# Optimization experiments

Hardware: AMD Instinct MI355X
Metric: run time of the kernel (lower is better)

Reference implementation:

```python
import jax, jax.numpy as jnp
import numpy as np

H = 768
NH = 12
HD = H // NH
NDIM = 5
LN_EPS = 1e-5


def setup_inputs() -> dict:
    key = jax.random.key(0)
    ks = jax.random.split(key, 12)
    B, S = 4, 2048
    xavier = lambda k: jax.random.uniform(k, (H, H), jnp.float32, -1.0, 1.0) * np.sqrt(6.0 / (H + H))
    return {
        "hidden_states": jax.random.normal(ks[0], (B, S, H), jnp.float32),
        "Wq": xavier(ks[1]), "bq": jnp.zeros((H,), jnp.float32),
        "Wk": xavier(ks[2]), "bk": jnp.zeros((H,), jnp.float32),
        "Wv": xavier(ks[3]), "bv": jnp.zeros((H,), jnp.float32),
        "Wo": xavier(ks[4]), "bo": jnp.zeros((H,), jnp.float32),
        # per-dimension, per-head scalar biases (torch init: zeros; use small randn so grads are non-trivial)
        "dim_biases": 0.02 * jax.random.normal(ks[5], (NDIM, NH), jnp.float32),
        "ln_gamma": jnp.ones((H,), jnp.float32),
        "ln_beta": jnp.zeros((H,), jnp.float32),
        "attention_mask": jax.random.randint(ks[6], (4, 2048), 0, 2, jnp.int32),
        "dimension_idx": 2,
    }


def reference(hidden_states, Wq, bq, Wk, bk, Wv, bv, Wo, bo, dim_biases,
              ln_gamma, ln_beta, attention_mask, dimension_idx):
    B, S, _ = hidden_states.shape
    residual = hidden_states
    # torch nn.Linear: x @ W.T + b
    q = (hidden_states @ Wq.T + bq).reshape(B, S, NH, HD).transpose(0, 2, 1, 3)  # [B,NH,S,HD]
    k = (hidden_states @ Wk.T + bk).reshape(B, S, NH, HD).transpose(0, 2, 1, 3)
    v = (hidden_states @ Wv.T + bv).reshape(B, S, NH, HD).transpose(0, 2, 1, 3)

    scores = jnp.einsum("bhqd,bhkd->bhqk", q, k) / np.sqrt(HD)  # [B,NH,S,S]
    if dimension_idx is not None and dimension_idx < NDIM:
        scores = scores + dim_biases[dimension_idx][None, :, None, None]
    # mask over key positions, broadcast over heads and queries
    scores = jnp.where(attention_mask[:, None, None, :] == 0, -jnp.inf, scores)
    attn = jax.nn.softmax(scores, axis=-1)

    ctx = jnp.einsum("bhqk,bhkd->bhqd", attn, v)  # [B,NH,S,HD]
    ctx = ctx.transpose(0, 2, 1, 3).reshape(B, S, H)
    out = ctx @ Wo.T + bo

    y = out + residual
    mu = jnp.mean(y, axis=-1, keepdims=True)
    var = jnp.var(y, axis=-1, keepdims=True)
    y = (y - mu) / jnp.sqrt(var + LN_EPS) * ln_gamma + ln_beta
    return y
```

## Files before the change

kernel.cpp:

```cpp
#include <hip/hip_runtime.h>
#include <hip/hip_bf16.h>

#define HH    768
#define NHEAD 12
#define HDIM  64
#define BB    4
#define SS    2048
#define MM    (BB*SS)
#define NDIMS 5
#define WEL   (HH*HH)
#define LOG2E 1.44269504088896f
#define QSCALE 0.180336881f

typedef unsigned short u16;
typedef __attribute__((ext_vector_type(8))) short short8;
typedef __attribute__((ext_vector_type(4))) float floatx4;
typedef __attribute__((ext_vector_type(16))) float floatx16;
typedef __attribute__((ext_vector_type(4))) unsigned int uint4v;
typedef __attribute__((ext_vector_type(2))) unsigned int uint2v;

__device__ __forceinline__ float bf2f(u16 u) {
    return __uint_as_float(((unsigned int)u) << 16);
}
__device__ __forceinline__ u16 f2bf(float f) {
    unsigned int x = __float_as_uint(f);
    unsigned int r = (x + 0x7fffu + ((x >> 16) & 1u)) >> 16;
    return (u16)r;
}
__device__ __forceinline__ unsigned int pack_bf16x2(float a, float b) {
    float2 f2 = make_float2(a, b);
    __hip_bfloat162 h2 = __float22bfloat162_rn(f2);
    return *reinterpret_cast<unsigned int*>(&h2);
}
__device__ __forceinline__ void gld16(const u16* g, u16* l) {
    __builtin_amdgcn_global_load_lds(
        (const __attribute__((address_space(1))) unsigned int*)g,
        (__attribute__((address_space(3))) unsigned int*)l, 16, 0, 0);
}

__global__ __launch_bounds__(256) void f32_to_bf16(
    const float* __restrict__ in, u16* __restrict__ out, int n8)
{
    int i = blockIdx.x * 256 + threadIdx.x;
    if (i >= n8) return;
    float4 a = ((const float4*)in)[i*2];
    float4 b = ((const float4*)in)[i*2 + 1];
    ushort4 lo, hi;
    lo.x = f2bf(a.x); lo.y = f2bf(a.y); lo.z = f2bf(a.z); lo.w = f2bf(a.w);
    hi.x = f2bf(b.x); hi.y = f2bf(b.y); hi.z = f2bf(b.z); hi.w = f2bf(b.w);
    ((ushort4*)out)[i*2]     = lo;
    ((ushort4*)out)[i*2 + 1] = hi;
}

#define XCVT_BLKS ((MM*HH)/8/256)
#define WCVT_BLKS (WEL/8/256)
__global__ __launch_bounds__(256) void cvt_all(
    const float* __restrict__ x,
    const float* __restrict__ W0, const float* __restrict__ W1,
    const float* __restrict__ W2, const float* __restrict__ W3,
    u16* __restrict__ xb, u16* __restrict__ wb)
{
    const int bid = blockIdx.x;
    const float* src;
    u16* dst;
    int i;
    if (bid < XCVT_BLKS) {
        src = x; dst = xb; i = bid * 256 + threadIdx.x;
    } else {
        const int wsel = (bid - XCVT_BLKS) / WCVT_BLKS;
        src = (wsel == 0) ? W0 : (wsel == 1) ? W1 : (wsel == 2) ? W2 : W3;
        dst = wb + (size_t)wsel * WEL;
        i = ((bid - XCVT_BLKS) % WCVT_BLKS) * 256 + threadIdx.x;
    }
    float4 a = ((const float4*)src)[i*2];
    float4 b = ((const float4*)src)[i*2 + 1];
    ushort4 lo, hi;
    lo.x = f2bf(a.x); lo.y = f2bf(a.y); lo.z = f2bf(a.z); lo.w = f2bf(a.w);
    hi.x = f2bf(b.x); hi.y = f2bf(b.y); hi.z = f2bf(b.z); hi.w = f2bf(b.w);
    ((ushort4*)dst)[i*2]     = lo;
    ((ushort4*)dst)[i*2 + 1] = hi;
}

__global__ __launch_bounds__(256) void v_transpose(
    const u16* __restrict__ V, u16* __restrict__ vt)
{
    __shared__ unsigned Ls[64][36];
    const int t = threadIdx.x;
    const int kt = blockIdx.x, h = blockIdx.y, b = blockIdx.z;
    const int p  = t & 31;
    const int dg = (t >> 5) * 8;
    const u16* va = V + ((size_t)(b*SS + kt*64 + 2*p))*HH + h*HDIM + dg;
    const u16* vb = va + HH;
    uint4 A = *(const uint4*)va;
    uint4 Bv = *(const uint4*)vb;
    const unsigned* Aw = (const unsigned*)&A;
    const unsigned* Bw = (const unsigned*)&Bv;
    #pragma unroll
    for (int i = 0; i < 4; ++i) {
        unsigned a = Aw[i], c = Bw[i];
        Ls[dg + 2*i][p]     = (a & 0xffffu) | (c << 16);
        Ls[dg + 2*i + 1][p] = (a >> 16) | (c & 0xffff0000u);
    }
    __syncthreads();
    const int d = t >> 2, kc = (t & 3) * 8;
    uint4 o0 = *(const uint4*)&Ls[d][kc];
    uint4 o1 = *(const uint4*)&Ls[d][kc + 4];
    u16* dst = vt + ((size_t)((b*NHEAD + h)*HDIM + d))*SS + kt*64 + kc*2;
    *(uint4*)dst       = o0;
    *(uint4*)(dst + 8) = o1;
}

__global__ __launch_bounds__(256, 3) void gemm_gld_qkv(
    const u16* __restrict__ Xb, const u16* __restrict__ Wb3,
    const float* __restrict__ bq, const float* __restrict__ bk, const float* __restrict__ bv,
    u16* __restrict__ oq, u16* __restrict__ ok, u16* __restrict__ vt)
{
    __shared__ u16 Xs[128][64];
    __shared__ u16 Ws[192][64];
    const int t = threadIdx.x;
    const int w = t >> 6, lane = t & 63;
    const int wy = w >> 1, wx = w & 1;
    const int m = lane & 31, hh = lane >> 5;
    const int grow = lane >> 3;
    const int cg   = (lane & 7) ^ grow;

    const int flat = blockIdx.x + 12 * blockIdx.y;
    const int swz  = (flat & 7) * 96 + (flat >> 3);
    const int j0 = (swz % 12) * 192;
    const int i0 = (swz / 12) * 128;
    const int sel = j0 / HH;
    const int lj  = j0 - sel * HH;
    const float* biasL = ((sel == 0) ? bq : (sel == 1) ? bk : bv) + lj;
    const u16* Wrows = Wb3 + (size_t)j0 * HH;

    floatx16 acc[2][3];
    #pragma unroll
    for (int am = 0; am < 2; ++am)
        #pragma unroll
        for (int bn = 0; bn < 3; ++bn)
            #pragma unroll
            for (int r = 0; r < 16; ++r) acc[am][bn][r] = 0.f;

    if (sel != 2) {
        for (int k0 = 0; k0 < HH; k0 += 64) {
            __syncthreads();
            #pragma unroll
            for (int j = 0; j < 4; ++j) {
                const int r = w*32 + j*8;
                gld16(Xb + (size_t)(i0 + r + grow)*HH + k0 + cg*8, &Xs[r][0]);
            }
            #pragma unroll
            for (int j = 0; j < 6; ++j) {
                const int r = w*48 + j*8;
                gld16(Wrows + (size_t)(r + grow)*HH + k0 + cg*8, &Ws[r][0]);
            }
            __syncthreads();

            #pragma unroll
            for (int kh = 0; kh < 4; ++kh) {
                const int ch = kh*2 + hh;
                short8 af[2], bf[3];
                #pragma unroll
                for (int am = 0; am < 2; ++am)
                    af[am] = *(const short8*)&Xs[wy*64 + am*32 + m][(ch ^ (m & 7))*8];
                #pragma unroll
                for (int bn = 0; bn < 3; ++bn)
                    bf[bn] = *(const short8*)&Ws[wx*96 + bn*32 + m][(ch ^ (m & 7))*8];
                #pragma unroll
                for (int am = 0; am < 2; ++am)
                    #pragma unroll
                    for (int bn = 0; bn < 3; ++bn)
                        acc[am][bn] = __builtin_amdgcn_mfma_f32_32x32x16_bf16(
                            af[am], bf[bn], acc[am][bn], 0, 0, 0);
            }
        }

        u16* outL = ((sel == 0) ? oq : ok) + lj;
        float bb[3];
        #pragma unroll
        for (int bn = 0; bn < 3; ++bn) bb[bn] = biasL[wx*96 + bn*32 + m];
        #pragma unroll
        for (int am = 0; am < 2; ++am)
            #pragma unroll
            for (int bn = 0; bn < 3; ++bn)
                #pragma unroll
                for (int r = 0; r < 16; ++r) {
                    int row = i0 + wy*64 + am*32 + (r & 3) + 8*(r >> 2) + 4*hh;
                    outL[(size_t)row*HH + wx*96 + bn*32 + m] = f2bf(acc[am][bn][r] + bb[bn]);
                }
    } else {
        for (int k0 = 0; k0 < HH; k0 += 64) {
            __syncthreads();
            #pragma unroll
            for (int j = 0; j < 4; ++j) {
                const int r = w*32 + j*8;
                gld16(Xb + (size_t)(i0 + r + grow)*HH + k0 + cg*8, &Xs[r][0]);
            }
            #pragma unroll
            for (int j = 0; j < 6; ++j) {
                const int r = w*48 + j*8;
                gld16(Wrows + (size_t)(r + grow)*HH + k0 + cg*8, &Ws[r][0]);
            }
            __syncthreads();

            #pragma unroll
            for (int kh = 0; kh < 4; ++kh) {
                const int ch = kh*2 + hh;
                short8 af[2], bf[3];
                #pragma unroll
                for (int am = 0; am < 2; ++am)
                    af[am] = *(const short8*)&Xs[wy*64 + am*32 + m][(ch ^ (m & 7))*8];
                #pragma unroll
                for (int bn = 0; bn < 3; ++bn)
                    bf[bn] = *(const short8*)&Ws[wx*96 + bn*32 + m][(ch ^ (m & 7))*8];
                #pragma unroll
                for (int am = 0; am < 2; ++am)
                    #pragma unroll
                    for (int bn = 0; bn < 3; ++bn)
                        acc[am][bn] = __builtin_amdgcn_mfma_f32_32x32x16_bf16(
                            bf[bn], af[am], acc[am][bn], 0, 0, 0);
            }
        }

        const int b_ = i0 / SS;
        const int key0 = (i0 % SS) + wy*64 + m;
        #pragma unroll
        for (int am = 0; am < 2; ++am)
            #pragma unroll
            for (int bn = 0; bn < 3; ++bn)
                #pragma unroll
                for (int qq = 0; qq < 4; ++qq) {
                    float4 bv4 = *(const float4*)&biasL[wx*96 + bn*32 + qq*8 + 4*hh];
                    const float* bvp = (const float*)&bv4;
                    #pragma unroll
                    for (int j = 0; j < 4; ++j) {
                        const int r = qq*4 + j;
                        const int wcol = wx*96 + bn*32 + qq*8 + 4*hh + j;
                        vt[(size_t)(b_*HH + lj + wcol)*SS + key0 + am*32] =
                            f2bf(acc[am][bn][r] + bvp[j]);
                    }
                }
    }
}

__global__ __launch_bounds__(256) void gemm_gld_m64(
    const u16* __restrict__ Xb, const u16* __restrict__ Wb,
    const float* __restrict__ bias, u16* __restrict__ out)
{
    __shared__ u16 Xs[64][64];
    __shared__ u16 Ws[128][64];
    const int t = threadIdx.x;
    const int w = t >> 6, lane = t & 63;
    const int m = lane & 31, hh = lane >> 5;
    const int grow = lane >> 3;
    const int cg   = (lane & 7) ^ grow;

    const int flat = blockIdx.x + 6 * blockIdx.y;
    const int swz  = (flat & 7) * 96 + (flat >> 3);
    const int j0 = (swz % 6) * 128;
    const int i0 = (swz / 6) * 64;

    floatx16 acc[2];
    #pragma unroll
    for (int am = 0; am < 2; ++am)
        #pragma unroll
        for (int r = 0; r < 16; ++r) acc[am][r] = 0.f;

    for (int k0 = 0; k0 < HH; k0 += 64) {
        __syncthreads();
        #pragma unroll
        for (int j = 0; j < 2; ++j) {
            const int r = w*16 + j*8;
            gld16(Xb + (size_t)(i0 + r + grow)*HH + k0 + cg*8, &Xs[r][0]);
        }
        #pragma unroll
        for (int j = 0; j < 4; ++j) {
            const int r = w*32 + j*8;
            gld16(Wb + (size_t)(j0 + r + grow)*HH + k0 + cg*8, &Ws[r][0]);
        }
        __syncthreads();

        #pragma unroll
        for (int kh = 0; kh < 4; ++kh) {
            const int ch = kh*2 + hh;
            short8 af[2], bf;
            af[0] = *(const short8*)&Xs[m][(ch ^ (m & 7))*8];
            af[1] = *(const short8*)&Xs[32 + m][(ch ^ (m & 7))*8];
            bf    = *(const short8*)&Ws[w*32 + m][(ch ^ (m & 7))*8];
            acc[0] = __builtin_amdgcn_mfma_f32_32x32x16_bf16(af[0], bf, acc[0], 0, 0, 0);
            acc[1] = __builtin_amdgcn_mfma_f32_32x32x16_bf16(af[1], bf, acc[1], 0, 0, 0);
        }
    }

    const float bb = bias[j0 + w*32 + m];
    #pragma unroll
    for (int am = 0; am < 2; ++am)
        #pragma unroll
        for (int r = 0; r < 16; ++r) {
            int row = i0 + am*32 + (r & 3) + 8*(r >> 2) + 4*hh;
            out[(size_t)row*HH + j0 + w*32 + m] = f2bf(acc[am][r] + bb);
        }
}

__global__ __launch_bounds__(256) void gemm_mfma_nt(
    const u16* __restrict__ Xb, const float* __restrict__ W,
    const float* __restrict__ bias, u16* __restrict__ out)
{
    __shared__ u16 Xs[128][40];
    __shared__ u16 Wt[64][40];
    const int t = threadIdx.x;
    const int w = t >> 6, lane = t & 63;
    const int c = lane & 15, qd = lane >> 4;
    const int i0 = blockIdx.y * 128, j0 = blockIdx.x * 64;
    const int xrow = t >> 1, xoff = (t & 1) * 16;
    const int wn = t >> 2, woff = (t & 3) * 8;

    floatx4 acc[2][4];
    #pragma unroll
    for (int mt = 0; mt < 2; ++mt)
        #pragma unroll
        for (int nt = 0; nt < 4; ++nt) acc[mt][nt] = (floatx4){0.f,0.f,0.f,0.f};

    for (int k0 = 0; k0 < HH; k0 += 32) {
        uint4 xa  = *(const uint4*)(Xb + (size_t)(i0 + xrow)*HH + k0 + xoff);
        uint4 xb2 = *(const uint4*)(Xb + (size_t)(i0 + xrow)*HH + k0 + xoff + 8);
        float4 wa = *(const float4*)(W + (size_t)(j0 + wn)*HH + k0 + woff);
        float4 wb = *(const float4*)(W + (size_t)(j0 + wn)*HH + k0 + woff + 4);
        __syncthreads();
        *(uint4*)&Xs[xrow][xoff]     = xa;
        *(uint4*)&Xs[xrow][xoff + 8] = xb2;
        ushort4 w0, w1;
        w0.x = f2bf(wa.x); w0.y = f2bf(wa.y); w0.z = f2bf(wa.z); w0.w = f2bf(wa.w);
        w1.x = f2bf(wb.x); w1.y = f2bf(wb.y); w1.z = f2bf(wb.z); w1.w = f2bf(wb.w);
        *(ushort4*)&Wt[wn][woff]     = w0;
        *(ushort4*)&Wt[wn][woff + 4] = w1;
        __syncthreads();

        short8 a0 = *(const short8*)&Xs[w*32 + c][qd*8];
        short8 a1 = *(const short8*)&Xs[w*32 + 16 + c][qd*8];
        #pragma unroll
        for (int nt = 0; nt < 4; ++nt) {
            short8 bfr = *(const short8*)&Wt[nt*16 + c][qd*8];
            acc[0][nt] = __builtin_amdgcn_mfma_f32_16x16x32_bf16(a0, bfr, acc[0][nt], 0, 0, 0);
            acc[1][nt] = __builtin_amdgcn_mfma_f32_16x16x32_bf16(a1, bfr, acc[1][nt], 0, 0, 0);
        }
    }

    float bv[4];
    #pragma unroll
    for (int nt = 0; nt < 4; ++nt) bv[nt] = bias[j0 + nt*16 + c];
    #pragma unroll
    for (int mt = 0; mt < 2; ++mt)
        #pragma unroll
        for (int nt = 0; nt < 4; ++nt)
            #pragma unroll
            for (int r = 0; r < 4; ++r)
                out[(size_t)(i0 + w*32 + mt*16 + qd*4 + r)*HH + j0 + nt*16 + c] =
                    f2bf(acc[mt][nt][r] + bv[nt]);
}

__global__ __launch_bounds__(256, 3) void attn_mfma32(
    const u16* __restrict__ Q, const u16* __restrict__ K, const u16* __restrict__ vt,
    const float* __restrict__ dim_biases, const int* __restrict__ mask,
    const int* __restrict__ dim_idx_p, u16* __restrict__ ctx)
{
    __shared__ u16 Ks[2][64][64];
    __shared__ u16 Vs[2][64][64];
    __shared__ float madd[2][64];

    const int t = threadIdx.x;
    const int w = t >> 6, lane = t & 63;
    const int ql = lane & 31, hi = lane >> 5;
    const int sw7 = ql & 7;

    const int flat = blockIdx.x + 16 * (blockIdx.y + 12 * blockIdx.z);
    const int swz  = (flat & 7) * 96 + (flat >> 3);
    const int q0 = (swz & 15) * 128;
    const int h  = (swz >> 4) % NHEAD;
    const int b  = swz / (16 * NHEAD);

    const int didx = *dim_idx_p;
    const float db2 = ((didx < NDIMS) ? dim_biases[didx*NHEAD + h] : 0.f) * LOG2E;

    const int grow = lane >> 3;
    const int cg   = (lane & 7) ^ grow;

    const u16* Vrows = vt + (size_t)(b*NHEAD + h)*HDIM*SS;

    short8 ones;
    #pragma unroll
    for (int j = 0; j < 8; ++j) ones[j] = (short)0x3F80;

    short8 qv[4];
    {
        const u16* qsrc = Q + ((size_t)(b*SS + q0 + w*32 + ql))*HH + h*HDIM + 8*hi;
        #pragma unroll
        for (int s = 0; s < 4; ++s) {
            ushort4 u0 = *(const ushort4*)(qsrc + s*16);
            ushort4 u1 = *(const ushort4*)(qsrc + s*16 + 4);
            const u16 uu[8] = {u0.x,u0.y,u0.z,u0.w,u1.x,u1.y,u1.z,u1.w};
            #pragma unroll
            for (int j = 0; j < 8; ++j)
                qv[s][j] = (short)f2bf(bf2f(uu[j]) * QSCALE);
        }
    }

    floatx16 o[2], lacc;
    #pragma unroll
    for (int r = 0; r < 16; ++r) { o[0][r] = 0.f; o[1][r] = 0.f; lacc[r] = 0.f; }

    int mreg = 0;

    auto issueKV = [&](int kt, int buf) {
        #pragma unroll
        for (int j = 0; j < 2; ++j) {
            const int rbase = w*16 + j*8;
            gld16(K + (size_t)(b*SS + kt*64 + rbase + grow)*HH + h*HDIM + cg*8,
                  &Ks[buf][rbase][0]);
            gld16(Vrows + (size_t)(rbase + grow)*SS + kt*64 + cg*8,
                  &Vs[buf][rbase][0]);
        }
    };
    auto issueM = [&](int kt) {
        if (t < 64) mreg = mask[(size_t)b*SS + kt*64 + t];
    };
    auto writeM = [&](int buf) {
        if (t < 64) madd[buf][t] = (mreg != 0) ? db2 : -1e30f;
    };

    issueKV(0, 0);
    issueM(0);
    writeM(0);

    for (int kt = 0; kt < SS/64; ++kt) {
        const int cur = kt & 1;
        __syncthreads();
        const bool more = (kt + 1 < SS/64);
        if (more) { issueKV(kt + 1, cur ^ 1); issueM(kt + 1); }

        #pragma unroll
        for (int kblk = 0; kblk < 2; ++kblk) {
            const u16* kb = &Ks[cur][kblk*32 + ql][0];

            floatx16 z;
            #pragma unroll
            for (int qq = 0; qq < 4; ++qq) {
                float4 mv = *(const float4*)&madd[cur][kblk*32 + qq*8 + 4*hi];
                z[qq*4+0] = mv.x; z[qq*4+1] = mv.y; z[qq*4+2] = mv.z; z[qq*4+3] = mv.w;
            }
            short8 kf[4];
            #pragma unroll
            for (int s = 0; s < 4; ++s)
                kf[s] = *(const short8*)(kb + ((s*2 + hi) ^ sw7)*8);
            __builtin_amdgcn_s_setprio(1);
            #pragma unroll
            for (int s = 0; s < 4; ++s)
                z = __builtin_amdgcn_mfma_f32_32x32x16_bf16(kf[s], qv[s], z, 0, 0, 0);
            __builtin_amdgcn_s_setprio(0);

            #pragma unroll
            for (int r = 0; r < 16; ++r) z[r] = __builtin_amdgcn_exp2f(z[r]);

            #pragma unroll
            for (int ks = 0; ks < 2; ++ks) {
                unsigned x0 = pack_bf16x2(z[ks*8 + 0], z[ks*8 + 1]);
                unsigned y0 = pack_bf16x2(z[ks*8 + 4], z[ks*8 + 5]);
                unsigned x1 = pack_bf16x2(z[ks*8 + 2], z[ks*8 + 3]);
                unsigned y1 = pack_bf16x2(z[ks*8 + 6], z[ks*8 + 7]);
                uint2v s0 = __builtin_amdgcn_permlane32_swap(x0, y0, false, false);
                uint2v s1 = __builtin_amdgcn_permlane32_swap(x1, y1, false, false);
                uint4v pv; pv[0] = s0[0]; pv[1] = s1[0]; pv[2] = s0[1]; pv[3] = s1[1];
                short8 pa = __builtin_bit_cast(short8, pv);

                const int ck = kblk*4 + ks*2 + hi;
                short8 vf0 = *(const short8*)&Vs[cur][ql][(ck ^ sw7)*8];
                short8 vf1 = *(const short8*)&Vs[cur][32 + ql][(ck ^ sw7)*8];

                __builtin_amdgcn_s_setprio(1);
                lacc = __builtin_amdgcn_mfma_f32_32x32x16_bf16(pa, ones, lacc, 0, 0, 0);
                o[0] = __builtin_amdgcn_mfma_f32_32x32x16_bf16(pa, vf0, o[0], 0, 0, 0);
                o[1] = __builtin_amdgcn_mfma_f32_32x32x16_bf16(pa, vf1, o[1], 0, 0, 0);
                __builtin_amdgcn_s_setprio(0);
            }
        }

        if (more) writeM(cur ^ 1);
    }

    #pragma unroll
    for (int r = 0; r < 16; ++r) {
        float l = lacc[r];
        float inv = (l > 0.f) ? 1.f / l : 0.f;
        const int qrow = q0 + w*32 + (r & 3) + 8*(r >> 2) + 4*hi;
        u16* dst = ctx + ((size_t)(b*SS + qrow))*HH + h*HDIM + ql;
        dst[0]  = f2bf(o[0][r] * inv);
        dst[32] = f2bf(o[1][r] * inv);
    }
}

__global__ __launch_bounds__(256) void add_ln_wave(
    const u16* __restrict__ proj, const float* __restrict__ resid,
    const float* __restrict__ gamma, const float* __restrict__ beta,
    float* __restrict__ out)
{
    const int t = threadIdx.x, w = t >> 6, lane = t & 63;
    const int row = blockIdx.x * 4 + w;
    const size_t base = (size_t)row * HH + lane * 12;
    const int gbase = lane * 12;

    float x[12];
    #pragma unroll
    for (int j = 0; j < 3; ++j) {
        ushort4 p = *(const ushort4*)(proj + base + j*4);
        float4  r = *(const float4*)(resid + base + j*4);
        x[j*4+0] = bf2f(p.x) + r.x;
        x[j*4+1] = bf2f(p.y) + r.y;
        x[j*4+2] = bf2f(p.z) + r.z;
        x[j*4+3] = bf2f(p.w) + r.w;
    }
    float s = 0.f, ss = 0.f;
    #pragma unroll
    for (int j = 0; j < 12; ++j) { s += x[j]; ss += x[j]*x[j]; }
    #pragma unroll
    for (int off = 1; off < 64; off <<= 1) {
        s  += __shfl_xor(s, off);
        ss += __shfl_xor(ss, off);
    }
    float mean = s * (1.f/768.f);
    float var  = ss * (1.f/768.f) - mean*mean;
    float rstd = rsqrtf(fmaxf(var, 0.f) + 1e-5f);
    #pragma unroll
    for (int j = 0; j < 3; ++j) {
        float4 g = *(const float4*)(gamma + gbase + j*4);
        float4 bt = *(const float4*)(beta + gbase + j*4);
        float4 y;
        y.x = (x[j*4+0]-mean)*rstd*g.x + bt.x;
        y.y = (x[j*4+1]-mean)*rstd*g.y + bt.y;
        y.z = (x[j*4+2]-mean)*rstd*g.z + bt.z;
        y.w = (x[j*4+3]-mean)*rstd*g.w + bt.w;
        *(float4*)(out + base + j*4) = y;
    }
}

extern "C" void kernel_launch(void* const* d_in, const int* in_sizes, int n_in,
                              void* d_out, int out_size, void* d_ws, size_t ws_size,
                              hipStream_t stream)
{
    (void)in_sizes; (void)n_in; (void)out_size;
    const float* x    = (const float*)d_in[0];
    const float* Wq   = (const float*)d_in[1];
    const float* bq   = (const float*)d_in[2];
    const float* Wk   = (const float*)d_in[3];
    const float* bk   = (const float*)d_in[4];
    const float* Wv   = (const float*)d_in[5];
    const float* bv   = (const float*)d_in[6];
    const float* Wo   = (const float*)d_in[7];
    const float* bo   = (const float*)d_in[8];
    const float* dimb = (const float*)d_in[9];
    const float* gam  = (const float*)d_in[10];
    const float* bet  = (const float*)d_in[11];
    const int* mask   = (const int*)d_in[12];
    const int* didx   = (const int*)d_in[13];

    const size_t N = (size_t)MM * HH;
    if (ws_size < 4 * N * sizeof(u16)) return;
    u16* ws = (u16*)d_ws;
    u16* q    = ws;
    u16* kbuf = ws + N;
    u16* vtb  = ws + 2*N;
    u16* slot3 = ws + 3*N;
    u16* xb   = slot3;
    u16* ctx  = slot3;
    u16* proj = q;

    const bool bigws = ws_size >= (4 * N + 4 * (size_t)WEL) * sizeof(u16);
    u16* wb = ws + 4 * N;

    if (bigws) {
        cvt_all<<<XCVT_BLKS + 4*WCVT_BLKS, 256, 0, stream>>>(x, Wq, Wk, Wv, Wo, xb, wb);
        gemm_gld_qkv<<<dim3(3*HH/192, MM/128), 256, 0, stream>>>(
            xb, wb, bq, bk, bv, q, kbuf, vtb);
        attn_mfma32<<<dim3(SS/128, NHEAD, BB), 256, 0, stream>>>(q, kbuf, vtb, dimb, mask, didx, ctx);
        gemm_gld_m64<<<dim3(HH/128, MM/64), 256, 0, stream>>>(ctx, wb + 3*WEL, bo, proj);
    } else {
        f32_to_bf16<<<(int)(N/8/256), 256, 0, stream>>>(x, xb, (int)(N/8));
        dim3 gg(HH/64, MM/128);
        gemm_mfma_nt<<<gg, 256, 0, stream>>>(xb, Wq, bq, q);
        gemm_mfma_nt<<<gg, 256, 0, stream>>>(xb, Wk, bk, kbuf);
        gemm_mfma_nt<<<gg, 256, 0, stream>>>(xb, Wv, bv, vtb);
        v_transpose<<<dim3(SS/64, NHEAD, BB), 256, 0, stream>>>(vtb, slot3);
        attn_mfma32<<<dim3(SS/128, NHEAD, BB), 256, 0, stream>>>(q, kbuf, slot3, dimb, mask, didx, vtb);
        gemm_mfma_nt<<<dim3(HH/64, MM/128), 256, 0, stream>>>(vtb, Wo, bo, proj);
    }
    add_ln_wave<<<MM/4, 256, 0, stream>>>(proj, x, gam, bet, (float*)d_out);
}
```

Baseline: 237.0 us.

## Fuse residual-add LayerNorm into output projection via last-block-per-row-tile counter

Folds the separate add+LayerNorm kernel into the output-projection GEMM. Each row tile of 64 rows is covered by 6 column blocks, and each block bumps an atomic counter. The last block to finish re-reads the bf16 projection and the residual and performs the LayerNorm for those 64 rows. This removes one kernel launch and a separate pass over the data, at the cost of a memset, threadfences, and a serialized LN tail in one block per row tile. The counters reuse the no-longer-needed K buffer.

```diff
diff --git a/kernel.cpp b/kernel.cpp
--- a/kernel.cpp
+++ b/kernel.cpp
@@ -243,12 +243,16 @@
     }
 }
 
-__global__ __launch_bounds__(256) void gemm_gld_m64(
+__global__ __launch_bounds__(256) void gemm_gld_m64_ln(
     const u16* __restrict__ Xb, const u16* __restrict__ Wb,
-    const float* __restrict__ bias, u16* __restrict__ out)
+    const float* __restrict__ bias, u16* __restrict__ proj,
+    const float* __restrict__ resid, const float* __restrict__ gamma,
+    const float* __restrict__ beta, float* __restrict__ lnout,
+    unsigned* __restrict__ counters)
 {
     __shared__ u16 Xs[64][64];
     __shared__ u16 Ws[128][64];
+    __shared__ int lastflag;
     const int t = threadIdx.x;
     const int w = t >> 6, lane = t & 63;
     const int m = lane & 31, hh = lane >> 5;
@@ -298,8 +302,61 @@
         #pragma unroll
         for (int r = 0; r < 16; ++r) {
             int row = i0 + am*32 + (r & 3) + 8*(r >> 2) + 4*hh;
-            out[(size_t)row*HH + j0 + w*32 + m] = f2bf(acc[am][r] + bb);
-        }
+            proj[(size_t)row*HH + j0 + w*32 + m] = f2bf(acc[am][r] + bb);
+        }
+
+    __threadfence();
+    __syncthreads();
+    if (t == 0)
+        lastflag = (atomicAdd(&counters[i0 >> 6], 1u) == 5u);
+    __syncthreads();
+    if (!lastflag) return;
+    __threadfence();
+
+    const int gbase = lane * 12;
+    float gv[12], bt[12];
+    #pragma unroll
+    for (int j = 0; j < 3; ++j) {
+        float4 g4 = *(const float4*)(gamma + gbase + j*4);
+        float4 b4 = *(const float4*)(beta  + gbase + j*4);
+        gv[j*4+0]=g4.x; gv[j*4+1]=g4.y; gv[j*4+2]=g4.z; gv[j*4+3]=g4.w;
+        bt[j*4+0]=b4.x; bt[j*4+1]=b4.y; bt[j*4+2]=b4.z; bt[j*4+3]=b4.w;
+    }
+
+    for (int rr = 0; rr < 16; ++rr) {
+        const int row = i0 + w*16 + rr;
+        const size_t base = (size_t)row * HH + lane * 12;
+        float x[12];
+        #pragma unroll
+        for (int j = 0; j < 3; ++j) {
+            ushort4 p = *(const ushort4*)(proj + base + j*4);
+            float4  r4 = *(const float4*)(resid + base + j*4);
+            x[j*4+0] = bf2f(p.x) + r4.x;
+            x[j*4+1] = bf2f(p.y) + r4.y;
+            x[j*4+2] = bf2f(p.z) + r4.z;
+            x[j*4+3] = bf2f(p.w) + r4.w;
+        }
+        float s = 0.f, ss = 0.f;
+        #pragma unroll
+        for (int j = 0; j < 12; ++j) { s += x[j]; ss += x[j]*x[j]; }
+        #pragma unroll
+        for (int off = 1; off < 64; off <<= 1) {
+            s  += __shfl_xor(s, off);
+            ss += __shfl_xor(ss, off);
+        }
+        float mean = s * (1.f/768.f);
+        float var  = ss * (1.f/768.f) - mean*mean;
+        float rstd = rsqrtf(fmaxf(var, 0.f) + 1e-5f);
+        #pragma unroll
+        for (int j = 0; j < 3; ++j) {
+            float4 y;
+            y.x = (x[j*4+0]-mean)*rstd*gv[j*4+0] + bt[j*4+0];
+            y.y = (x[j*4+1]-mean)*rstd*gv[j*4+1] + bt[j*4+1];
+            y.z = (x[j*4+2]-mean)*rstd*gv[j*4+2] + bt[j*4+2];
+            y.w = (x[j*4+3]-mean)*rstd*gv[j*4+3] + bt[j*4+3];
+            *(float4*)(lnout + base + j*4) = y;
+        }
+    }
 }
 
 __global__ __launch_bounds__(256) void gemm_mfma_nt(
@@ -581,7 +638,9 @@
         gemm_gld_qkv<<<dim3(3*HH/192, MM/128), 256, 0, stream>>>(
             xb, wb, bq, bk, bv, q, kbuf, vtb);
         attn_mfma32<<<dim3(SS/128, NHEAD, BB), 256, 0, stream>>>(q, kbuf, vtb, dimb, mask, didx, ctx);
-        gemm_gld_m64<<<dim3(HH/128, MM/64), 256, 0, stream>>>(ctx, wb + 3*WEL, bo, proj);
+        hipMemsetAsync((void*)kbuf, 0, 128 * sizeof(unsigned), stream);
+        gemm_gld_m64_ln<<<dim3(HH/128, MM/64), 256, 0, stream>>>(
+            ctx, wb + 3*WEL, bo, proj, x, gam, bet, (float*)d_out, (unsigned*)kbuf);
     } else {
         f32_to_bf16<<<(int)(N/8/256), 256, 0, stream>>>(x, xb, (int)(N/8));
         dim3 gg(HH/64, MM/128);
@@ -591,6 +650,6 @@
         v_transpose<<<dim3(SS/64, NHEAD, BB), 256, 0, stream>>>(vtb, slot3);
         attn_mfma32<<<dim3(SS/128, NHEAD, BB), 256, 0, stream>>>(q, kbuf, slot3, dimb, mask, didx, vtb);
         gemm_mfma_nt<<<dim3(HH/64, MM/128), 256, 0, stream>>>(vtb, Wo, bo, proj);
-    }
-    add_ln_wave<<<MM/4, 256, 0, stream>>>(proj, x, gam, bet, (float*)d_out);
-}
+        add_ln_wave<<<MM/4, 256, 0, stream>>>(proj, x, gam, bet, (float*)d_out);
+    }
+}
```

Result: slower. 344.2 us (+45.2%).
